# Performance work log

Hardware: AMD Instinct MI355X
Metric: run time of the kernel (lower is better)

## Reference

```python
import jax, jax.numpy as jnp
import numpy as np

B, IN, OUT, G = 64, 8192, 8192, 64
NG = IN // G  # groups per row


def setup_inputs() -> dict:
    key = jax.random.key(0)
    k1, k2, k3, k4 = jax.random.split(key, 4)
    x = jax.random.normal(k1, (B, IN), dtype=jnp.float32)
    # packed 2-bit codes: 4 codes per byte, LSB-first (matches _pack2)
    w_packed = jax.random.randint(k2, (OUT, IN // 4), 0, 256, dtype=jnp.int32).astype(jnp.uint8)
    # scales from _calc_group_qparams are positive (max_abs/1.5); zp is always 2
    scales = jax.random.uniform(k3, (OUT, NG), dtype=jnp.float32, minval=0.01, maxval=0.1)
    zps = jnp.full((OUT, NG), 2, dtype=jnp.int32)
    bias = jax.random.normal(k4, (OUT,), dtype=jnp.float32) * 0.01
    return {"x": x, "w_packed": w_packed, "scales": scales, "zps": zps, "bias": bias}


def _dequant(w_packed, scales, zps):
    # unpack: byte -> 4 two-bit codes, LSB first (matches _unpack2)
    out_f = w_packed.shape[0]
    codes = jnp.stack([(w_packed >> s) & 3 for s in (0, 2, 4, 6)], axis=-1)  # [OUT, IN//4, 4]
    q = codes.reshape(out_f, NG, G).astype(jnp.int32)                        # [OUT, NG, G]
    # per-group dequant: (q - zp) * scale
    w = (q - zps[:, :, None]).astype(jnp.float32) * scales[:, :, None]
    return w.reshape(out_f, IN)                                              # [OUT, IN]


def reference(x, w_packed, scales, zps, bias):
    w = _dequant(w_packed, scales, zps)  # [OUT, IN] fp32
    # original accumulates xg @ wg.T per group; equivalent to full x @ w.T
    return x @ w.T + bias                # [B, OUT]
```

## Files before the change

### kernel.cpp

```cpp
#include <hip/hip_runtime.h>
#include <hip/hip_bf16.h>

#define B_    64
#define IN_   8192
#define OUT_  8192
#define NG_   128
#define PB_   2048
#define KSPLIT 16
#define KC    512

typedef float f32x4 __attribute__((ext_vector_type(4)));
typedef short s16x8 __attribute__((ext_vector_type(8)));
typedef _Float16 f16x4 __attribute__((ext_vector_type(4)));

#define OFF_WQ   (1u << 20)
#define OFF_TAB  (17u << 20)
#define OFF_PART (25u << 20)
#define OFF_FLAG (41u << 20)

__global__ __launch_bounds__(256) void k_flag(const unsigned* __restrict__ wp,
                                              int* __restrict__ flag) {
    __shared__ int f;
    unsigned any = 0;
#pragma unroll
    for (int i = 0; i < 16; ++i)
        any |= (wp[i * 256 + threadIdx.x] > 255u) ? 1u : 0u;
    if (threadIdx.x == 0) f = 0;
    __syncthreads();
    if (any) f = 1;
    __syncthreads();
    if (threadIdx.x == 0) *flag = f;
}

__global__ __launch_bounds__(256) void k_wpack(const unsigned char* __restrict__ wp,
                                               unsigned char* __restrict__ wq,
                                               const int* __restrict__ flag) {
    const int c  = threadIdx.x >> 4;
    const int r  = blockIdx.x * 16 + (threadIdx.x & 15);
    uint4 v[8];
    if (*flag) {
        const uint4* src = (const uint4*)(wp + r * PB_ + c * 128);
#pragma unroll
        for (int u = 0; u < 8; ++u) v[u] = src[u];
    } else {
        const int* src = (const int*)wp + r * PB_ + c * 128;
#pragma unroll
        for (int u = 0; u < 8; ++u) {
            unsigned d[4];
#pragma unroll
            for (int w = 0; w < 4; ++w) {
                const int* p = src + u * 16 + w * 4;
                d[w] = (unsigned)(p[0] & 0xFF) | ((unsigned)(p[1] & 0xFF) << 8) |
                       ((unsigned)(p[2] & 0xFF) << 16) | ((unsigned)(p[3] & 0xFF) << 24);
            }
            v[u] = (uint4){d[0], d[1], d[2], d[3]};
        }
    }
    uint4* dst = (uint4*)(wq + ((unsigned)c * OUT_ + r) * 128);
#pragma unroll
    for (int u = 0; u < 8; ++u) dst[u] = v[u];
}

__global__ __launch_bounds__(256) void k_spack(const float* __restrict__ scales,
                                               const int* __restrict__ zps,
                                               uint2* __restrict__ tab) {
    const int e = blockIdx.x * 256 + threadIdx.x;
    const int n = e >> 7, g = e & 127;
    const float s = scales[e];
    const float zf = (float)zps[e];
    const float v0 = -zf * s, v1 = v0 + s, v2 = v1 + s, v3 = v2 + s;
    __hip_bfloat162 lo = __float22bfloat162_rn(make_float2(v0, v1));
    __hip_bfloat162 hi = __float22bfloat162_rn(make_float2(v2, v3));
    uint2 ent; ent.x = *(unsigned*)&lo; ent.y = *(unsigned*)&hi;
    tab[(((unsigned)(g >> 3) * OUT_) + n) * 8 + (g & 7)] = ent;
}

__global__ __launch_bounds__(256) void k_pre(const float* __restrict__ x,
                                             uint4* __restrict__ xfrag) {
    const int kidx = blockIdx.x >> 2;
    const int part = blockIdx.x & 3;
#pragma unroll
    for (int i = 0; i < 4; ++i) {
        const int idx = (part * 4 + i) * 256 + threadIdx.x;
        const int sg = idx >> 6, lane = idx & 63;
        const int tt = sg >> 2, mt = sg & 3;
        const int sb = tt >> 2, b = tt & 3;
        const int q = lane >> 4, nn = lane & 15;
        const float* src = x + (mt * 16 + nn) * IN_ + kidx * KC + q * 128 + sb * 32 + b * 8;
        const float4 f0 = *(const float4*)src;
        const float4 f1 = *(const float4*)(src + 4);
        __hip_bfloat162 h0 = __float22bfloat162_rn(make_float2(f0.x, f0.y));
        __hip_bfloat162 h1 = __float22bfloat162_rn(make_float2(f0.z, f0.w));
        __hip_bfloat162 h2 = __float22bfloat162_rn(make_float2(f1.x, f1.y));
        __hip_bfloat162 h3 = __float22bfloat162_rn(make_float2(f1.z, f1.w));
        uint4 o;
        o.x = *(unsigned*)&h0; o.y = *(unsigned*)&h1;
        o.z = *(unsigned*)&h2; o.w = *(unsigned*)&h3;
        xfrag[kidx * 4096 + idx] = o;
    }
}

__global__ __launch_bounds__(256, 2) void k_main(
    const uint4* __restrict__ xfrag,
    const unsigned char* __restrict__ wq,
    const uint4* __restrict__ tab,
    _Float16* __restrict__ part)
{
    __shared__ uint4 x_lds[4096];

    const int tid  = threadIdx.x;
    const int wave = tid >> 6;
    const int lane = tid & 63;
    const int q    = lane >> 4;
    const int nn   = lane & 15;

    const int kidx    = blockIdx.x & (KSPLIT - 1);
    const int nblk    = blockIdx.x >> 4;
    const int colbase = nblk * 256 + wave * 64;

    uint4 w4[4][2];
#pragma unroll
    for (int cg = 0; cg < 4; ++cg) {
        const unsigned n = colbase + cg * 16 + nn;
        const uint4* src = (const uint4*)(wq + ((unsigned)kidx * OUT_ + n) * 128 + q * 32);
        w4[cg][0] = src[0];
        w4[cg][1] = src[1];
    }
    uint4 tq[4];
#pragma unroll
    for (int cg = 0; cg < 4; ++cg) {
        const unsigned n = colbase + cg * 16 + nn;
        tq[cg] = tab[((unsigned)kidx * OUT_ + n) * 4 + q];
    }
#pragma unroll
    for (int i = 0; i < 16; ++i) {
        const int sg = wave * 16 + i;
        const uint4* src = xfrag + kidx * 4096 + sg * 64 + lane;
        __builtin_amdgcn_global_load_lds(
            (const __attribute__((address_space(1))) unsigned int*)src,
            (__attribute__((address_space(3))) unsigned int*)
                ((char*)x_lds + sg * 1024),
            16, 0, 0);
    }
    __syncthreads();

    f32x4 acc[4][4];
#pragma unroll
    for (int cg = 0; cg < 4; ++cg)
#pragma unroll
        for (int mt = 0; mt < 4; ++mt)
            acc[cg][mt] = (f32x4){0.f, 0.f, 0.f, 0.f};

#pragma unroll
    for (int sb = 0; sb < 4; ++sb) {
#pragma unroll
        for (int b = 0; b < 4; ++b) {
            const int t = sb * 4 + b;
            union { uint4 u4; s16x8 s8; } av[4];
#pragma unroll
            for (int mt = 0; mt < 4; ++mt)
                av[mt].u4 = x_lds[(t * 4 + mt) * 64 + lane];
#pragma unroll
            for (int cg = 0; cg < 4; ++cg) {
                const uint4 ch = w4[cg][sb >> 1];
                const unsigned dwv =
                    ((const unsigned*)&ch)[((sb & 1) << 1) | (b >> 1)];
                const unsigned u = (b & 1) ? (dwv >> 16) : (dwv & 0xFFFFu);
                const unsigned tl = (sb >> 1) ? tq[cg].z : tq[cg].x;
                const unsigned th = (sb >> 1) ? tq[cg].w : tq[cg].y;
                union { unsigned w[4]; s16x8 s8; } bf;
#pragma unroll
                for (int m = 0; m < 4; ++m) {
                    const unsigned c0 = (u >> (4 * m)) & 3u;
                    const unsigned c1 = (u >> (4 * m + 2)) & 3u;
                    const unsigned sel = (0x0100u + c0 * 0x0202u)
                                       | ((0x0100u + c1 * 0x0202u) << 16);
                    bf.w[m] = __builtin_amdgcn_perm(th, tl, sel);
                }
#pragma unroll
                for (int mt = 0; mt < 4; ++mt)
                    acc[cg][mt] = __builtin_amdgcn_mfma_f32_16x16x32_bf16(
                        av[mt].s8, bf.s8, acc[cg][mt], 0, 0, 0);
            }
        }
    }

    _Float16* pp = part + kidx * (B_ * OUT_);
#pragma unroll
    for (int cg = 0; cg < 4; ++cg) {
        const int col = colbase + cg * 16 + nn;
#pragma unroll
        for (int mt = 0; mt < 4; ++mt)
#pragma unroll
            for (int r = 0; r < 4; ++r)
                pp[(mt * 16 + q * 4 + r) * OUT_ + col] = (_Float16)acc[cg][mt][r];
    }
}

__global__ __launch_bounds__(256) void k_reduce(const _Float16* __restrict__ part,
                                                const float* __restrict__ bias,
                                                float* __restrict__ out) {
    const int gtid = blockIdx.x * 256 + threadIdx.x;
    const int b  = gtid >> 11;
    const int n0 = (gtid & 2047) * 4;
    float4 s = *(const float4*)(bias + n0);
#pragma unroll
    for (int p = 0; p < KSPLIT; ++p) {
        f16x4 v = *(const f16x4*)(part + p * (B_ * OUT_) + b * OUT_ + n0);
        s.x += (float)v[0]; s.y += (float)v[1];
        s.z += (float)v[2]; s.w += (float)v[3];
    }
    *(float4*)(out + b * OUT_ + n0) = s;
}

extern "C" void kernel_launch(void* const* d_in, const int* in_sizes, int n_in,
                              void* d_out, int out_size, void* d_ws, size_t ws_size,
                              hipStream_t stream) {
    const float*         x      = (const float*)d_in[0];
    const unsigned char* wp     = (const unsigned char*)d_in[1];
    const float*         scales = (const float*)d_in[2];
    const int*           zps    = (const int*)d_in[3];
    const float*         bias   = (const float*)d_in[4];
    float*               out    = (float*)d_out;

    char* ws = (char*)d_ws;
    uint4*          xfrag = (uint4*)ws;
    unsigned char*  wq    = (unsigned char*)(ws + OFF_WQ);
    uint4*          tab   = (uint4*)(ws + OFF_TAB);
    _Float16*       part  = (_Float16*)(ws + OFF_PART);
    int*            flag  = (int*)(ws + OFF_FLAG);

    k_flag<<<1, 256, 0, stream>>>((const unsigned*)wp, flag);
    k_wpack<<<512, 256, 0, stream>>>(wp, wq, flag);
    k_spack<<<4096, 256, 0, stream>>>(scales, zps, (uint2*)tab);
    k_pre<<<64, 256, 0, stream>>>(x, xfrag);
    k_main<<<512, 256, 0, stream>>>(xfrag, wq, tab, part);
    k_reduce<<<512, 256, 0, stream>>>(part, bias, out);
}
```

Baseline: 144.9 us.

## Fuse prep kernels, switch to 32x32 MFMA, and build dequant tables in-kernel

Merges the flag, weight-repack, scale-pack and x-conversion kernels into one k_prep launch, which removes several launches and the large per-group table write. It stores bf16 scales only and builds the four-entry dequant table inside k_main with a bit trick that assumes zp==2, falling back to a general path when any block reports a different zero point. The main kernel switches from 16x16x32 to 32x32x16 MFMA and splits the x and weight loads into two phases so the second half overlaps compute. The bit-trick table is less exact in rounding than the float version, and it adds per-block zero-point flag checks.

```diff
diff --git a/kernel.cpp b/kernel.cpp
--- a/kernel.cpp
+++ b/kernel.cpp
@@ -9,191 +9,244 @@
 #define KSPLIT 16
 #define KC    512
 
-typedef float f32x4 __attribute__((ext_vector_type(4)));
-typedef short s16x8 __attribute__((ext_vector_type(8)));
-typedef _Float16 f16x4 __attribute__((ext_vector_type(4)));
+typedef float    f32x16 __attribute__((ext_vector_type(16)));
+typedef short    s16x8  __attribute__((ext_vector_type(8)));
+typedef _Float16 f16x4  __attribute__((ext_vector_type(4)));
 
 #define OFF_WQ   (1u << 20)
-#define OFF_TAB  (17u << 20)
-#define OFF_PART (25u << 20)
-#define OFF_FLAG (41u << 20)
-
-__global__ __launch_bounds__(256) void k_flag(const unsigned* __restrict__ wp,
-                                              int* __restrict__ flag) {
-    __shared__ int f;
-    unsigned any = 0;
-#pragma unroll
-    for (int i = 0; i < 16; ++i)
-        any |= (wp[i * 256 + threadIdx.x] > 255u) ? 1u : 0u;
-    if (threadIdx.x == 0) f = 0;
-    __syncthreads();
-    if (any) f = 1;
-    __syncthreads();
-    if (threadIdx.x == 0) *flag = f;
-}
-
-__global__ __launch_bounds__(256) void k_wpack(const unsigned char* __restrict__ wp,
-                                               unsigned char* __restrict__ wq,
-                                               const int* __restrict__ flag) {
-    const int c  = threadIdx.x >> 4;
-    const int r  = blockIdx.x * 16 + (threadIdx.x & 15);
-    uint4 v[8];
-    if (*flag) {
-        const uint4* src = (const uint4*)(wp + r * PB_ + c * 128);
-#pragma unroll
-        for (int u = 0; u < 8; ++u) v[u] = src[u];
+#define OFF_SQ   (17u << 20)
+#define OFF_ZF   (19u << 20)
+#define OFF_PART (20u << 20)
+
+__global__ __launch_bounds__(256) void k_prep(
+    const float* __restrict__ x, const unsigned char* __restrict__ wp,
+    const float* __restrict__ scales, const int* __restrict__ zps,
+    uint4* __restrict__ xfrag, unsigned char* __restrict__ wq,
+    uint4* __restrict__ sq, int* __restrict__ zflags)
+{
+    __shared__ uint4 lds[2048];
+    __shared__ int zf;
+    const int bid = blockIdx.x, tid = threadIdx.x;
+
+    if (bid < 512) {
+        const unsigned v = ((const unsigned*)wp)[tid];
+        const bool u8mode = __any((int)(v > 255u));
+        if (u8mode) {
+            const uint4* src = (const uint4*)wp + bid * 2048;
+#pragma unroll
+            for (int i = 0; i < 8; ++i) lds[tid + i * 256] = src[tid + i * 256];
+        } else {
+            const int* src = (const int*)wp + bid * 32768;
+#pragma unroll
+            for (int i = 0; i < 8; ++i) {
+                const int j = tid + i * 256;
+                const int* p = src + j * 16;
+                unsigned d[4];
+#pragma unroll
+                for (int w = 0; w < 4; ++w)
+                    d[w] = (unsigned)(p[w*4] & 0xFF) | ((unsigned)(p[w*4+1] & 0xFF) << 8) |
+                           ((unsigned)(p[w*4+2] & 0xFF) << 16) | ((unsigned)(p[w*4+3] & 0xFF) << 24);
+                lds[j] = (uint4){d[0], d[1], d[2], d[3]};
+            }
+        }
+        __syncthreads();
+        const int c = tid >> 4, r = tid & 15;
+        uint4* dst = (uint4*)wq + ((unsigned)c * OUT_ + bid * 16 + r) * 8;
+#pragma unroll
+        for (int u = 0; u < 8; ++u) dst[u] = lds[r * 128 + c * 8 + u];
+    } else if (bid < 576) {
+        const int b2 = bid - 512;
+        const int kidx = b2 >> 2, prt = b2 & 3;
+#pragma unroll
+        for (int i = 0; i < 4; ++i) {
+            const int idx = prt * 1024 + i * 256 + tid;
+            const int sg = idx >> 6, lane = idx & 63;
+            const int t = sg >> 1, mt = sg & 1;
+            const int h = lane >> 5, m = lane & 31;
+            const float* src = x + (mt * 32 + m) * IN_ + kidx * KC + h * 256 + t * 8;
+            const float4 f0 = *(const float4*)src;
+            const float4 f1 = *(const float4*)(src + 4);
+            __hip_bfloat162 h0 = __float22bfloat162_rn(make_float2(f0.x, f0.y));
+            __hip_bfloat162 h1 = __float22bfloat162_rn(make_float2(f0.z, f0.w));
+            __hip_bfloat162 h2 = __float22bfloat162_rn(make_float2(f1.x, f1.y));
+            __hip_bfloat162 h3 = __float22bfloat162_rn(make_float2(f1.z, f1.w));
+            uint4 o;
+            o.x = *(unsigned*)&h0; o.y = *(unsigned*)&h1;
+            o.z = *(unsigned*)&h2; o.w = *(unsigned*)&h3;
+            xfrag[kidx * 4096 + idx] = o;
+        }
     } else {
-        const int* src = (const int*)wp + r * PB_ + c * 128;
-#pragma unroll
-        for (int u = 0; u < 8; ++u) {
-            unsigned d[4];
-#pragma unroll
-            for (int w = 0; w < 4; ++w) {
-                const int* p = src + u * 16 + w * 4;
-                d[w] = (unsigned)(p[0] & 0xFF) | ((unsigned)(p[1] & 0xFF) << 8) |
-                       ((unsigned)(p[2] & 0xFF) << 16) | ((unsigned)(p[3] & 0xFF) << 24);
-            }
-            v[u] = (uint4){d[0], d[1], d[2], d[3]};
-        }
-    }
-    uint4* dst = (uint4*)(wq + ((unsigned)c * OUT_ + r) * 128);
-#pragma unroll
-    for (int u = 0; u < 8; ++u) dst[u] = v[u];
-}
-
-__global__ __launch_bounds__(256) void k_spack(const float* __restrict__ scales,
-                                               const int* __restrict__ zps,
-                                               uint2* __restrict__ tab) {
-    const int e = blockIdx.x * 256 + threadIdx.x;
-    const int n = e >> 7, g = e & 127;
-    const float s = scales[e];
-    const float zf = (float)zps[e];
-    const float v0 = -zf * s, v1 = v0 + s, v2 = v1 + s, v3 = v2 + s;
-    __hip_bfloat162 lo = __float22bfloat162_rn(make_float2(v0, v1));
-    __hip_bfloat162 hi = __float22bfloat162_rn(make_float2(v2, v3));
-    uint2 ent; ent.x = *(unsigned*)&lo; ent.y = *(unsigned*)&hi;
-    tab[(((unsigned)(g >> 3) * OUT_) + n) * 8 + (g & 7)] = ent;
-}
-
-__global__ __launch_bounds__(256) void k_pre(const float* __restrict__ x,
-                                             uint4* __restrict__ xfrag) {
-    const int kidx = blockIdx.x >> 2;
-    const int part = blockIdx.x & 3;
-#pragma unroll
-    for (int i = 0; i < 4; ++i) {
-        const int idx = (part * 4 + i) * 256 + threadIdx.x;
-        const int sg = idx >> 6, lane = idx & 63;
-        const int tt = sg >> 2, mt = sg & 3;
-        const int sb = tt >> 2, b = tt & 3;
-        const int q = lane >> 4, nn = lane & 15;
-        const float* src = x + (mt * 16 + nn) * IN_ + kidx * KC + q * 128 + sb * 32 + b * 8;
-        const float4 f0 = *(const float4*)src;
-        const float4 f1 = *(const float4*)(src + 4);
-        __hip_bfloat162 h0 = __float22bfloat162_rn(make_float2(f0.x, f0.y));
-        __hip_bfloat162 h1 = __float22bfloat162_rn(make_float2(f0.z, f0.w));
-        __hip_bfloat162 h2 = __float22bfloat162_rn(make_float2(f1.x, f1.y));
-        __hip_bfloat162 h3 = __float22bfloat162_rn(make_float2(f1.z, f1.w));
-        uint4 o;
-        o.x = *(unsigned*)&h0; o.y = *(unsigned*)&h1;
-        o.z = *(unsigned*)&h2; o.w = *(unsigned*)&h3;
-        xfrag[kidx * 4096 + idx] = o;
+        const int b3 = bid - 576;
+        if (tid < 128) {
+            const int n = b3 * 128 + tid;
+#pragma unroll
+            for (int kidx = 0; kidx < 16; ++kidx) {
+                const float* sp = scales + n * NG_ + kidx * 8;
+                const float4 s0 = *(const float4*)sp;
+                const float4 s1 = *(const float4*)(sp + 4);
+                __hip_bfloat162 h0 = __float22bfloat162_rn(make_float2(s0.x, s0.y));
+                __hip_bfloat162 h1 = __float22bfloat162_rn(make_float2(s0.z, s0.w));
+                __hip_bfloat162 h2 = __float22bfloat162_rn(make_float2(s1.x, s1.y));
+                __hip_bfloat162 h3 = __float22bfloat162_rn(make_float2(s1.z, s1.w));
+                uint4 o;
+                o.x = *(unsigned*)&h0; o.y = *(unsigned*)&h1;
+                o.z = *(unsigned*)&h2; o.w = *(unsigned*)&h3;
+                sq[(unsigned)kidx * OUT_ + n] = o;
+            }
+        }
+        if (tid == 0) zf = 0;
+        __syncthreads();
+        int bad = 0;
+        const int4* zp4 = (const int4*)zps + b3 * 4096;
+#pragma unroll
+        for (int i = 0; i < 16; ++i) {
+            const int4 z = zp4[i * 256 + tid];
+            bad |= (z.x != 2) | (z.y != 2) | (z.z != 2) | (z.w != 2);
+        }
+        if (bad) zf = 1;
+        __syncthreads();
+        if (tid == 0) zflags[b3] = zf;
     }
 }
 
 __global__ __launch_bounds__(256, 2) void k_main(
-    const uint4* __restrict__ xfrag,
-    const unsigned char* __restrict__ wq,
-    const uint4* __restrict__ tab,
-    _Float16* __restrict__ part)
+    const uint4* __restrict__ xfrag, const unsigned char* __restrict__ wq,
+    const uint2* __restrict__ sq2, const int* __restrict__ zflags,
+    const int* __restrict__ zps, _Float16* __restrict__ part)
 {
     __shared__ uint4 x_lds[4096];
 
-    const int tid  = threadIdx.x;
-    const int wave = tid >> 6;
-    const int lane = tid & 63;
-    const int q    = lane >> 4;
-    const int nn   = lane & 15;
-
-    const int kidx    = blockIdx.x & (KSPLIT - 1);
-    const int nblk    = blockIdx.x >> 4;
+    const int tid = threadIdx.x, wave = tid >> 6, lane = tid & 63;
+    const int h = lane >> 5, n32 = lane & 31;
+    const int kidx = blockIdx.x & (KSPLIT - 1);
+    const int nblk = blockIdx.x >> 4;
     const int colbase = nblk * 256 + wave * 64;
 
-    uint4 w4[4][2];
-#pragma unroll
-    for (int cg = 0; cg < 4; ++cg) {
-        const unsigned n = colbase + cg * 16 + nn;
-        const uint4* src = (const uint4*)(wq + ((unsigned)kidx * OUT_ + n) * 128 + q * 32);
-        w4[cg][0] = src[0];
-        w4[cg][1] = src[1];
-    }
-    uint4 tq[4];
-#pragma unroll
-    for (int cg = 0; cg < 4; ++cg) {
-        const unsigned n = colbase + cg * 16 + nn;
-        tq[cg] = tab[((unsigned)kidx * OUT_ + n) * 4 + q];
-    }
-#pragma unroll
-    for (int i = 0; i < 16; ++i) {
-        const int sg = wave * 16 + i;
+    uint4 w[2][4];
+    uint2 sv[2];
+    int ncol[2];
+#pragma unroll
+    for (int cg = 0; cg < 2; ++cg) {
+        const int n = colbase + cg * 32 + n32;
+        ncol[cg] = n;
+        const uint4* wb = (const uint4*)(wq + ((unsigned)kidx * OUT_ + n) * 128 + h * 64);
+        w[cg][0] = wb[0];
+        w[cg][1] = wb[1];
+        sv[cg] = sq2[((unsigned)kidx * OUT_ + n) * 2 + h];
+    }
+    const int zv = zflags[lane & 63];
+#pragma unroll
+    for (int i = 0; i < 8; ++i) {
+        const int sg = wave * 8 + i;
         const uint4* src = xfrag + kidx * 4096 + sg * 64 + lane;
         __builtin_amdgcn_global_load_lds(
-            (const __attribute__((address_space(1))) unsigned int*)src,
-            (__attribute__((address_space(3))) unsigned int*)
-                ((char*)x_lds + sg * 1024),
+            (const __attribute__((address_space(1))) unsigned*)src,
+            (__attribute__((address_space(3))) unsigned*)((char*)x_lds + sg * 1024),
             16, 0, 0);
     }
+    const bool zgen = __any(zv != 0);
     __syncthreads();
 
-    f32x4 acc[4][4];
-#pragma unroll
-    for (int cg = 0; cg < 4; ++cg)
-#pragma unroll
-        for (int mt = 0; mt < 4; ++mt)
-            acc[cg][mt] = (f32x4){0.f, 0.f, 0.f, 0.f};
-
-#pragma unroll
-    for (int sb = 0; sb < 4; ++sb) {
-#pragma unroll
-        for (int b = 0; b < 4; ++b) {
-            const int t = sb * 4 + b;
-            union { uint4 u4; s16x8 s8; } av[4];
-#pragma unroll
-            for (int mt = 0; mt < 4; ++mt)
-                av[mt].u4 = x_lds[(t * 4 + mt) * 64 + lane];
-#pragma unroll
-            for (int cg = 0; cg < 4; ++cg) {
-                const uint4 ch = w4[cg][sb >> 1];
-                const unsigned dwv =
-                    ((const unsigned*)&ch)[((sb & 1) << 1) | (b >> 1)];
-                const unsigned u = (b & 1) ? (dwv >> 16) : (dwv & 0xFFFFu);
-                const unsigned tl = (sb >> 1) ? tq[cg].z : tq[cg].x;
-                const unsigned th = (sb >> 1) ? tq[cg].w : tq[cg].y;
-                union { unsigned w[4]; s16x8 s8; } bf;
-#pragma unroll
-                for (int m = 0; m < 4; ++m) {
-                    const unsigned c0 = (u >> (4 * m)) & 3u;
-                    const unsigned c1 = (u >> (4 * m + 2)) & 3u;
-                    const unsigned sel = (0x0100u + c0 * 0x0202u)
-                                       | ((0x0100u + c1 * 0x0202u) << 16);
-                    bf.w[m] = __builtin_amdgcn_perm(th, tl, sel);
+#pragma unroll
+    for (int cg = 0; cg < 2; ++cg) {
+        const uint4* wb = (const uint4*)(wq + ((unsigned)kidx * OUT_ + ncol[cg]) * 128 + h * 64);
+        w[cg][2] = wb[2];
+        w[cg][3] = wb[3];
+    }
+#pragma unroll
+    for (int i = 0; i < 8; ++i) {
+        const int sg = 32 + wave * 8 + i;
+        const uint4* src = xfrag + kidx * 4096 + sg * 64 + lane;
+        __builtin_amdgcn_global_load_lds(
+            (const __attribute__((address_space(1))) unsigned*)src,
+            (__attribute__((address_space(3))) unsigned*)((char*)x_lds + sg * 1024),
+            16, 0, 0);
+    }
+
+    unsigned tl[2][4], th[2][4];
+#pragma unroll
+    for (int cg = 0; cg < 2; ++cg) {
+#pragma unroll
+        for (int gg = 0; gg < 4; ++gg) {
+            const unsigned dwv = (gg >> 1) ? sv[cg].y : sv[cg].x;
+            const unsigned s16 = (gg & 1) ? (dwv >> 16) : (dwv & 0xFFFFu);
+            if (!zgen) {
+                const unsigned m1 = s16 | 0x8000u;
+                const unsigned m2 = (s16 + 0x0080u) | 0x8000u;
+                tl[cg][gg] = m2 | (m1 << 16);
+                th[cg][gg] = s16 << 16;
+            } else {
+                union { unsigned u; float f; } sf; sf.u = s16 << 16;
+                const int g = kidx * 8 + h * 4 + gg;
+                const float zf = (float)zps[ncol[cg] * NG_ + g];
+                const float v0 = (0.f - zf) * sf.f, v1 = (1.f - zf) * sf.f;
+                const float v2 = (2.f - zf) * sf.f, v3 = (3.f - zf) * sf.f;
+                __hip_bfloat162 lo = __float22bfloat162_rn(make_float2(v0, v1));
+                __hip_bfloat162 hi = __float22bfloat162_rn(make_float2(v2, v3));
+                tl[cg][gg] = *(unsigned*)&lo;
+                th[cg][gg] = *(unsigned*)&hi;
+            }
+        }
+    }
+
+    f32x16 acc[2][2];
+#pragma unroll
+    for (int cg = 0; cg < 2; ++cg)
+#pragma unroll
+        for (int mt = 0; mt < 2; ++mt)
+#pragma unroll
+            for (int r = 0; r < 16; ++r) acc[cg][mt][r] = 0.f;
+
+#pragma unroll
+    for (int p = 0; p < 2; ++p) {
+        if (p) __syncthreads();
+#pragma unroll
+        for (int t8 = 0; t8 < 2; ++t8) {
+#pragma unroll
+            for (int dw = 0; dw < 4; ++dw) {
+#pragma unroll
+                for (int hf = 0; hf < 2; ++hf) {
+                    const int t = p * 16 + t8 * 8 + dw * 2 + hf;
+                    union { uint4 u4; s16x8 s8; } av[2];
+#pragma unroll
+                    for (int mt = 0; mt < 2; ++mt)
+                        av[mt].u4 = x_lds[(t * 2 + mt) * 64 + lane];
+#pragma unroll
+                    for (int cg = 0; cg < 2; ++cg) {
+                        const uint4 wc = w[cg][p * 2 + t8];
+                        const unsigned wdw = ((const unsigned*)&wc)[dw];
+                        const unsigned u = hf ? (wdw >> 16) : (wdw & 0xFFFFu);
+                        const unsigned tlv = tl[cg][p * 2 + t8];
+                        const unsigned thv = th[cg][p * 2 + t8];
+                        union { unsigned w_[4]; s16x8 s8; } bf;
+#pragma unroll
+                        for (int m = 0; m < 4; ++m) {
+                            const unsigned c0 = (u >> (4 * m)) & 3u;
+                            const unsigned c1 = (u >> (4 * m + 2)) & 3u;
+                            const unsigned sel = 0x01000100u + c0 * 0x0202u + c1 * 0x02020000u;
+                            bf.w_[m] = __builtin_amdgcn_perm(thv, tlv, sel);
+                        }
+#pragma unroll
+                        for (int mt = 0; mt < 2; ++mt)
+                            acc[cg][mt] = __builtin_amdgcn_mfma_f32_32x32x16_bf16(
+                                av[mt].s8, bf.s8, acc[cg][mt], 0, 0, 0);
+                    }
                 }
-#pragma unroll
-                for (int mt = 0; mt < 4; ++mt)
-                    acc[cg][mt] = __builtin_amdgcn_mfma_f32_16x16x32_bf16(
-                        av[mt].s8, bf.s8, acc[cg][mt], 0, 0, 0);
             }
         }
     }
 
     _Float16* pp = part + kidx * (B_ * OUT_);
 #pragma unroll
-    for (int cg = 0; cg < 4; ++cg) {
-        const int col = colbase + cg * 16 + nn;
-#pragma unroll
-        for (int mt = 0; mt < 4; ++mt)
-#pragma unroll
-            for (int r = 0; r < 4; ++r)
-                pp[(mt * 16 + q * 4 + r) * OUT_ + col] = (_Float16)acc[cg][mt][r];
+    for (int cg = 0; cg < 2; ++cg) {
+        const int col = ncol[cg];
+#pragma unroll
+        for (int mt = 0; mt < 2; ++mt)
+#pragma unroll
+            for (int r = 0; r < 16; ++r) {
+                const int row = (r & 3) + 8 * (r >> 2) + 4 * h;
+                pp[(mt * 32 + row) * OUT_ + col] = (_Float16)acc[cg][mt][r];
+            }
     }
 }
 
@@ -206,7 +259,7 @@
     float4 s = *(const float4*)(bias + n0);
 #pragma unroll
     for (int p = 0; p < KSPLIT; ++p) {
-        f16x4 v = *(const f16x4*)(part + p * (B_ * OUT_) + b * OUT_ + n0);
+        const f16x4 v = *(const f16x4*)(part + p * (B_ * OUT_) + b * OUT_ + n0);
         s.x += (float)v[0]; s.y += (float)v[1];
         s.z += (float)v[2]; s.w += (float)v[3];
     }
@@ -224,16 +277,13 @@
     float*               out    = (float*)d_out;
 
     char* ws = (char*)d_ws;
-    uint4*          xfrag = (uint4*)ws;
-    unsigned char*  wq    = (unsigned char*)(ws + OFF_WQ);
-    uint4*          tab   = (uint4*)(ws + OFF_TAB);
-    _Float16*       part  = (_Float16*)(ws + OFF_PART);
-    int*            flag  = (int*)(ws + OFF_FLAG);
-
-    k_flag<<<1, 256, 0, stream>>>((const unsigned*)wp, flag);
-    k_wpack<<<512, 256, 0, stream>>>(wp, wq, flag);
-    k_spack<<<4096, 256, 0, stream>>>(scales, zps, (uint2*)tab);
-    k_pre<<<64, 256, 0, stream>>>(x, xfrag);
-    k_main<<<512, 256, 0, stream>>>(xfrag, wq, tab, part);
+    uint4*         xfrag = (uint4*)ws;
+    unsigned char* wq    = (unsigned char*)(ws + OFF_WQ);
+    uint4*         sq    = (uint4*)(ws + OFF_SQ);
+    int*           zfl   = (int*)(ws + OFF_ZF);
+    _Float16*      part  = (_Float16*)(ws + OFF_PART);
+
+    k_prep<<<640, 256, 0, stream>>>(x, wp, scales, zps, xfrag, wq, sq, zfl);
+    k_main<<<512, 256, 0, stream>>>(xfrag, wq, (const uint2*)sq, zfl, zps, part);
     k_reduce<<<512, 256, 0, stream>>>(part, bias, out);
 }
```

New measurement: 132.9 us. -8.3%, faster.
